# Optimization experiments

Hardware: AMD Instinct MI355X
Metric: run time of the kernel (lower is better)

The kernel has to match this reference:

```python
import jax, jax.numpy as jnp
import numpy as np

N, E, D, H, G = 50000, 800000, 128, 128, 64
EPS = 1e-5


def setup_inputs() -> dict:
    key = jax.random.key(0)
    ks = jax.random.split(key, 16)
    x = jax.random.normal(ks[0], (N, D), dtype=jnp.float32)
    edge_index = jax.random.randint(ks[1], (2, E), 0, N, dtype=jnp.int64)
    batch = jnp.sort(jax.random.randint(ks[2], (N,), 0, G, dtype=jnp.int64))
    dims = [D, H, H, H]
    params = {}
    for i in range(3):
        params[f"W{i}"] = jax.random.normal(ks[3 + i], (dims[i], dims[i + 1]), dtype=jnp.float32) * (1.0 / np.sqrt(dims[i]).astype(np.float32))
        params[f"b{i}"] = jnp.zeros((dims[i + 1],), jnp.float32)
        params[f"g{i}"] = jnp.ones((dims[i + 1],), jnp.float32)   # BN gamma
        params[f"be{i}"] = jnp.zeros((dims[i + 1],), jnp.float32)  # BN beta
    params["Wout"] = jax.random.normal(ks[10], (H, 1), dtype=jnp.float32) * (1.0 / np.sqrt(H).astype(np.float32))
    params["bout"] = jnp.zeros((1,), jnp.float32)
    return {"x": x, "edge_index": edge_index, "batch": batch, **params}


def _gcn_forward(x, edge_index, batch, Ws, bs, gs, bes, Wout, bout):
    n = x.shape[0]
    loop = jnp.arange(n)
    # GCNConv default: add self-loops, symmetric degree normalization
    src = jnp.concatenate([edge_index[0], loop])
    dst = jnp.concatenate([edge_index[1], loop])
    deg = jax.ops.segment_sum(jnp.ones_like(dst, x.dtype), dst, num_segments=n)
    dinv = jax.lax.rsqrt(jnp.maximum(deg, 1.0))  # deg >= 1 from self-loops
    norm = dinv[src] * dinv[dst]                 # [E+N]
    h = x
    for W, b, g, be in zip(Ws, bs, gs, bes):
        h = h @ W                                               # transform [N,C]
        msg = h[src] * norm[:, None]                            # gather [E+N,C]
        h = jax.ops.segment_sum(msg, dst, num_segments=n) + b   # scatter-add
        # BatchNorm1d (training-mode batch statistics over nodes)
        mu = jnp.mean(h, axis=0)
        var = jnp.var(h, axis=0)
        h = (h - mu) * jax.lax.rsqrt(var + EPS) * g + be
        h = jax.nn.relu(h)
        # dropout: identity (deterministic eval reference)
    counts = jax.ops.segment_sum(jnp.ones((n,), h.dtype), batch, num_segments=G)
    pooled = jax.ops.segment_sum(h, batch, num_segments=G) / jnp.maximum(counts, 1.0)[:, None]
    return jax.nn.sigmoid(pooled @ Wout + bout)  # [G,1]


def reference(x, edge_index, batch, W0, b0, g0, be0, W1, b1, g1, be1, W2, b2, g2, be2, Wout, bout):
    return _gcn_forward(x, edge_index, batch,
                        (W0, W1, W2), (b0, b1, b2), (g0, g1, g2), (be0, be1, be2),
                        Wout, bout)
```

## Files before the change

kernel.cpp:

```cpp
#include <hip/hip_runtime.h>

#define EPSBN 1e-5f
#define AGG_BLOCKS 2048

using bf16x8 = __attribute__((ext_vector_type(8))) short;
using f32x4  = __attribute__((ext_vector_type(4))) float;

__device__ __forceinline__ unsigned short f2bf(float f) {
    unsigned u = __builtin_bit_cast(unsigned, f);
    unsigned r = (u + 0x7FFFu + ((u >> 16) & 1u)) >> 16;
    return (unsigned short)r;
}
__device__ __forceinline__ float bf2f(unsigned short s) {
    unsigned u = ((unsigned)s) << 16;
    return __builtin_bit_cast(float, u);
}


__global__ __launch_bounds__(256) void k_bhist(const int* __restrict__ dst, int E,
                                               int* __restrict__ deg, int* __restrict__ bcnt, int shift) {
    __shared__ int lh[512];
    for (int i = threadIdx.x; i < 512; i += 256) lh[i] = 0;
    __syncthreads();
    for (int i = blockIdx.x * blockDim.x + threadIdx.x; i < E; i += gridDim.x * blockDim.x) {
        int d = dst[i];
        atomicAdd(&deg[d], 1);
        atomicAdd(&lh[d >> shift], 1);
    }
    __syncthreads();
    for (int i = threadIdx.x; i < 512; i += 256)
        if (lh[i]) atomicAdd(&bcnt[i], lh[i]);
}

__global__ void k_dinv(const int* __restrict__ deg, int N, float* __restrict__ dinv) {
    int i = blockIdx.x * blockDim.x + threadIdx.x;
    if (i < N) dinv[i] = rsqrtf((float)(deg[i] + 1));
}

__global__ void k_scan1(const int* __restrict__ deg, int N, int* __restrict__ rs, int* __restrict__ blk) {
    __shared__ int sh[256];
    int tid = threadIdx.x;
    int i = blockIdx.x * 256 + tid;
    int v = (i < N) ? deg[i] : 0;
    sh[tid] = v; __syncthreads();
    for (int off = 1; off < 256; off <<= 1) {
        int t = (tid >= off) ? sh[tid - off] : 0;
        __syncthreads();
        sh[tid] += t;
        __syncthreads();
    }
    if (i < N) rs[i] = sh[tid] - v;
    if (tid == 255) blk[blockIdx.x] = sh[255];
}

__global__ void k_scan2(const int* __restrict__ blk, int nb, int* __restrict__ blkoff) {
    __shared__ int sh[1024];
    int tid = threadIdx.x;
    int v = (tid < nb) ? blk[tid] : 0;
    sh[tid] = v; __syncthreads();
    for (int off = 1; off < 1024; off <<= 1) {
        int t = (tid >= off) ? sh[tid - off] : 0;
        __syncthreads();
        sh[tid] += t;
        __syncthreads();
    }
    if (tid < nb) blkoff[tid] = sh[tid] - v;
}

__global__ void k_scan3(int* __restrict__ rs, int N, const int* __restrict__ blkoff) {
    int i = blockIdx.x * blockDim.x + threadIdx.x;
    if (i < N) rs[i] += blkoff[i >> 8];
}


__global__ __launch_bounds__(256) void k_bscatter(const int* __restrict__ src, const int* __restrict__ dst, int E,
                                                  const int* __restrict__ boff, int* __restrict__ gcur,
                                                  uint2* __restrict__ ebuf, int shift) {
    __shared__ int lh[512], lb[512];
    int tid = threadIdx.x;
    int base = blockIdx.x * 2048;
    for (int i = tid; i < 512; i += 256) lh[i] = 0;
    __syncthreads();
    int ms[8], md[8];
    #pragma unroll
    for (int j = 0; j < 8; ++j) {
        int idx = base + j * 256 + tid;
        if (idx < E) {
            ms[j] = src[idx]; md[j] = dst[idx];
            atomicAdd(&lh[md[j] >> shift], 1);
        } else md[j] = -1;
    }
    __syncthreads();
    for (int b = tid; b < 512; b += 256) {
        int c = lh[b];
        lb[b] = c ? atomicAdd(&gcur[b], c) : 0;
    }
    __syncthreads();
    for (int i = tid; i < 512; i += 256) lh[i] = 0;
    __syncthreads();
    #pragma unroll
    for (int j = 0; j < 8; ++j) {
        if (md[j] >= 0) {
            int b = md[j] >> shift;
            int r = atomicAdd(&lh[b], 1);
            ebuf[boff[b] + lb[b] + r] = make_uint2((unsigned)ms[j], (unsigned)md[j]);
        }
    }
}


__global__ __launch_bounds__(256) void k_fill2(const uint2* __restrict__ ebuf, const int* __restrict__ bcnt,
                                               const int* __restrict__ boff, const int* __restrict__ rs,
                                               int* __restrict__ col, int shift) {
    __shared__ int lcur[256];
    int b = blockIdx.x;
    int n0 = b << shift;
    int cnt = bcnt[b], s = boff[b];
    int span = 1 << shift;
    for (int i = threadIdx.x; i < span; i += 256) lcur[i] = 0;
    __syncthreads();
    for (int i = threadIdx.x; i < cnt; i += 256) {
        uint2 e = ebuf[s + i];
        int d = (int)e.y;
        int pos = rs[d] + atomicAdd(&lcur[d - n0], 1);
        col[pos] = (int)e.x;
    }
}


__global__ __launch_bounds__(256) void k_gemm(const unsigned short* __restrict__ Abf,
                                              const float* __restrict__ Af,
                                              const float* __restrict__ W,
                                              unsigned short* __restrict__ C, int N,
                                              const float* __restrict__ scale,
                                              const float* __restrict__ shift, int mode) {
    __shared__ unsigned short Asw[128 * 128];
    __shared__ unsigned short Wt[128 * 128];
    int tid = threadIdx.x;
    int r0 = blockIdx.x * 128;

    {
        int n = tid & 127, kh = tid >> 7;
        const float* wp = &W[(kh * 64) * 128 + n];
        #pragma unroll
        for (int kb = 0; kb < 8; ++kb) {
            unsigned short t8[8];
            #pragma unroll
            for (int e = 0; e < 8; ++e)
                t8[e] = f2bf(wp[(kb * 8 + e) * 128]);
            int byte = (n * 256 + kh * 128 + kb * 16) ^ ((n & 7) << 4);
            *reinterpret_cast<uint4*>(reinterpret_cast<char*>(Wt) + byte) =
                *reinterpret_cast<const uint4*>(t8);
        }
    }
    if (mode == 0) {
        const float* ap = &Af[(size_t)r0 * 128];
        #pragma unroll
        for (int j = 0; j < 8; ++j) {
            int u = tid + j * 256;
            int row = u >> 4, cg = u & 15;
            unsigned short t8[8] = {0,0,0,0,0,0,0,0};
            if (r0 + row < N) {
                float4 a0 = *reinterpret_cast<const float4*>(ap + row * 128 + cg * 8);
                float4 a1 = *reinterpret_cast<const float4*>(ap + row * 128 + cg * 8 + 4);
                t8[0]=f2bf(a0.x); t8[1]=f2bf(a0.y); t8[2]=f2bf(a0.z); t8[3]=f2bf(a0.w);
                t8[4]=f2bf(a1.x); t8[5]=f2bf(a1.y); t8[6]=f2bf(a1.z); t8[7]=f2bf(a1.w);
            }
            int byte = (row * 256 + cg * 16) ^ ((row & 7) << 4);
            *reinterpret_cast<uint4*>(reinterpret_cast<char*>(Asw) + byte) =
                *reinterpret_cast<const uint4*>(t8);
        }
    } else {
        const unsigned short* ap = &Abf[(size_t)r0 * 128];
        #pragma unroll
        for (int j = 0; j < 8; ++j) {
            int u = tid + j * 256;
            int row = u >> 4, cg = u & 15;
            unsigned short t8[8] = {0,0,0,0,0,0,0,0};
            if (r0 + row < N) {
                ushort4 v0 = *reinterpret_cast<const ushort4*>(ap + (size_t)row * 128 + cg * 8);
                ushort4 v1 = *reinterpret_cast<const ushort4*>(ap + (size_t)row * 128 + cg * 8 + 4);
                float4 sc0 = *reinterpret_cast<const float4*>(&scale[cg * 8]);
                float4 sc1 = *reinterpret_cast<const float4*>(&scale[cg * 8 + 4]);
                float4 sf0 = *reinterpret_cast<const float4*>(&shift[cg * 8]);
                float4 sf1 = *reinterpret_cast<const float4*>(&shift[cg * 8 + 4]);
                t8[0] = f2bf(fmaxf(bf2f(v0.x) * sc0.x + sf0.x, 0.f));
                t8[1] = f2bf(fmaxf(bf2f(v0.y) * sc0.y + sf0.y, 0.f));
                t8[2] = f2bf(fmaxf(bf2f(v0.z) * sc0.z + sf0.z, 0.f));
                t8[3] = f2bf(fmaxf(bf2f(v0.w) * sc0.w + sf0.w, 0.f));
                t8[4] = f2bf(fmaxf(bf2f(v1.x) * sc1.x + sf1.x, 0.f));
                t8[5] = f2bf(fmaxf(bf2f(v1.y) * sc1.y + sf1.y, 0.f));
                t8[6] = f2bf(fmaxf(bf2f(v1.z) * sc1.z + sf1.z, 0.f));
                t8[7] = f2bf(fmaxf(bf2f(v1.w) * sc1.w + sf1.w, 0.f));
            }
            int byte = (row * 256 + cg * 16) ^ ((row & 7) << 4);
            *reinterpret_cast<uint4*>(reinterpret_cast<char*>(Asw) + byte) =
                *reinterpret_cast<const uint4*>(t8);
        }
    }
    __syncthreads();

    int wv = tid >> 6, lane = tid & 63;
    int lr = lane & 15, lk = lane >> 4;
    f32x4 acc[2][8] = {};
    #pragma unroll
    for (int kk = 0; kk < 4; ++kk) {
        bf16x8 af[2], bf[8];
        #pragma unroll
        for (int mf = 0; mf < 2; ++mf) {
            int ar = wv * 32 + mf * 16 + lr;
            int byte = (ar * 256 + kk * 64 + lk * 16) ^ ((ar & 7) << 4);
            af[mf] = *reinterpret_cast<const bf16x8*>(reinterpret_cast<const char*>(Asw) + byte);
        }
        #pragma unroll
        for (int nf = 0; nf < 8; ++nf) {
            int bn = nf * 16 + lr;
            int byte = (bn * 256 + kk * 64 + lk * 16) ^ ((bn & 7) << 4);
            bf[nf] = *reinterpret_cast<const bf16x8*>(reinterpret_cast<const char*>(Wt) + byte);
        }
        #pragma unroll
        for (int mf = 0; mf < 2; ++mf)
            #pragma unroll
            for (int nf = 0; nf < 8; ++nf)
                acc[mf][nf] = __builtin_amdgcn_mfma_f32_16x16x32_bf16(af[mf], bf[nf], acc[mf][nf], 0, 0, 0);
    }
    __syncthreads();
    #pragma unroll
    for (int mf = 0; mf < 2; ++mf)
        #pragma unroll
        for (int nf = 0; nf < 8; ++nf)
            #pragma unroll
            for (int r = 0; r < 4; ++r) {
                int row = wv * 32 + mf * 16 + lk * 4 + r;
                int colc = nf * 16 + lr;
                Asw[row * 128 + colc] = f2bf(acc[mf][nf][r]);
            }
    __syncthreads();
    #pragma unroll
    for (int j = 0; j < 8; ++j) {
        int u = tid + j * 256;
        int row = u >> 4, cg = u & 15;
        if (r0 + row < N)
            *reinterpret_cast<uint4*>(&C[((size_t)(r0 + row)) * 128 + cg * 8]) =
                *reinterpret_cast<const uint4*>(&Asw[row * 128 + cg * 8]);
    }
}


__global__ __launch_bounds__(256) void k_agg(const unsigned short* __restrict__ t, const int* __restrict__ col,
                                             const int* __restrict__ rs, const int* __restrict__ deg,
                                             const float* __restrict__ dinv, const float* __restrict__ bias,
                                             unsigned short* __restrict__ out, int N,
                                             float* __restrict__ p1, float* __restrict__ p2) {
    int wv = threadIdx.x >> 6, lane = threadIdx.x & 63;
    const ushort2* tp = reinterpret_cast<const ushort2*>(t);
    float b0 = bias[2 * lane], b1 = bias[2 * lane + 1];
    float s1x = 0.f, s1y = 0.f, s2x = 0.f, s2y = 0.f;
    for (int w = blockIdx.x * 4 + wv; w < N; w += gridDim.x * 4) {
        int start = rs[w], cnt = deg[w];
        float di = dinv[w];
        float ax = 0.f, ay = 0.f;
        int e = 0;
        for (; e + 4 <= cnt; e += 4) {
            int s0 = col[start + e], s1 = col[start + e + 1];
            int s2 = col[start + e + 2], s3 = col[start + e + 3];
            float w0 = dinv[s0], w1 = dinv[s1], w2 = dinv[s2], w3 = dinv[s3];
            ushort2 v0 = tp[(size_t)s0 * 64 + lane];
            ushort2 v1 = tp[(size_t)s1 * 64 + lane];
            ushort2 v2 = tp[(size_t)s2 * 64 + lane];
            ushort2 v3 = tp[(size_t)s3 * 64 + lane];
            ax += w0 * bf2f(v0.x) + w1 * bf2f(v1.x) + w2 * bf2f(v2.x) + w3 * bf2f(v3.x);
            ay += w0 * bf2f(v0.y) + w1 * bf2f(v1.y) + w2 * bf2f(v2.y) + w3 * bf2f(v3.y);
        }
        for (; e < cnt; ++e) {
            int s = col[start + e];
            float ww = dinv[s];
            ushort2 v = tp[(size_t)s * 64 + lane];
            ax += ww * bf2f(v.x);
            ay += ww * bf2f(v.y);
        }
        ushort2 self = tp[(size_t)w * 64 + lane];
        ushort2 o;
        o.x = f2bf(di * ax + di * di * bf2f(self.x) + b0);
        o.y = f2bf(di * ay + di * di * bf2f(self.y) + b1);
        reinterpret_cast<ushort2*>(out)[(size_t)w * 64 + lane] = o;
        float rx = bf2f(o.x), ry = bf2f(o.y);
        s1x += rx; s1y += ry; s2x += rx * rx; s2y += ry * ry;
    }
    __shared__ float sh[4][64][4];
    sh[wv][lane][0] = s1x; sh[wv][lane][1] = s1y; sh[wv][lane][2] = s2x; sh[wv][lane][3] = s2y;
    __syncthreads();
    int tid = threadIdx.x;
    if (tid < 64) {
        float a0 = 0.f, a1 = 0.f, a2 = 0.f, a3 = 0.f;
        #pragma unroll
        for (int r = 0; r < 4; ++r) {
            a0 += sh[r][tid][0]; a1 += sh[r][tid][1];
            a2 += sh[r][tid][2]; a3 += sh[r][tid][3];
        }
        p1[blockIdx.x * 128 + 2 * tid]     = a0;
        p1[blockIdx.x * 128 + 2 * tid + 1] = a1;
        p2[blockIdx.x * 128 + 2 * tid]     = a2;
        p2[blockIdx.x * 128 + 2 * tid + 1] = a3;
    }
}


__global__ __launch_bounds__(128) void k_statsmid(const float* __restrict__ p1, const float* __restrict__ p2,
                                                  int rows, float* __restrict__ pm1, float* __restrict__ pm2) {
    int c = threadIdx.x, b = blockIdx.x;
    int r0 = b * rows;
    float s1 = 0.f, s2 = 0.f;
    #pragma unroll 4
    for (int r = 0; r < rows; ++r) {
        s1 += p1[(size_t)(r0 + r) * 128 + c];
        s2 += p2[(size_t)(r0 + r) * 128 + c];
    }
    pm1[b * 128 + c] = s1;
    pm2[b * 128 + c] = s2;
}

__global__ __launch_bounds__(1024) void k_stats2(const float* __restrict__ p1, const float* __restrict__ p2,
                                                 int nb, int N,
                                                 const float* __restrict__ g, const float* __restrict__ be,
                                                 float* __restrict__ scale, float* __restrict__ shift) {
    __shared__ double sh1[1024], sh2[1024];
    int tid = threadIdx.x;
    int c = tid & 127, seg = tid >> 7;
    double s1 = 0.0, s2 = 0.0;
    int b = seg;
    for (; b + 32 <= nb; b += 32) {
        double a0 = p1[(b      ) * 128 + c], q0 = p2[(b      ) * 128 + c];
        double a1 = p1[(b +  8) * 128 + c], q1 = p2[(b +  8) * 128 + c];
        double a2 = p1[(b + 16) * 128 + c], q2 = p2[(b + 16) * 128 + c];
        double a3 = p1[(b + 24) * 128 + c], q3 = p2[(b + 24) * 128 + c];
        s1 += (a0 + a1) + (a2 + a3);
        s2 += (q0 + q1) + (q2 + q3);
    }
    for (; b < nb; b += 8) { s1 += p1[b * 128 + c]; s2 += p2[b * 128 + c]; }
    sh1[tid] = s1; sh2[tid] = s2;
    __syncthreads();
    #pragma unroll
    for (int s = 4; s >= 1; s >>= 1) {
        if (seg < s) {
            sh1[tid] += sh1[tid + s * 128];
            sh2[tid] += sh2[tid + s * 128];
        }
        __syncthreads();
    }
    if (tid < 128) {
        double mu = sh1[c] / N;
        double var = sh2[c] / N - mu * mu;
        double inv = 1.0 / sqrt(var + (double)EPSBN);
        scale[c] = (float)((double)g[c] * inv);
        shift[c] = (float)((double)be[c] - mu * (double)g[c] * inv);
    }
}


__global__ __launch_bounds__(256) void k_pool(const unsigned short* __restrict__ h, const int* __restrict__ batch,
                                              const float* __restrict__ scale, const float* __restrict__ shift,
                                              const float* __restrict__ Wout, int N, int G,
                                              float* __restrict__ pool, int* __restrict__ cnt) {
    __shared__ float pl[64];
    __shared__ int cl[64];
    int tid = threadIdx.x;
    if (tid < 64) { pl[tid] = 0.f; cl[tid] = 0; }
    __syncthreads();
    int wv = tid >> 6, lane = tid & 63;
    float sc0 = scale[2 * lane], sc1 = scale[2 * lane + 1];
    float sf0 = shift[2 * lane], sf1 = shift[2 * lane + 1];
    float w0 = Wout[2 * lane], w1 = Wout[2 * lane + 1];
    const ushort2* hp = reinterpret_cast<const ushort2*>(h);
    int wid = blockIdx.x * 4 + wv;
    int stride = gridDim.x * 4;
    for (int i = wid; i < N; i += stride * 4) {
        int i1 = i + stride, i2 = i + 2 * stride, i3 = i + 3 * stride;
        float s0 = 0.f, s1 = 0.f, s2 = 0.f, s3 = 0.f;
        {
            ushort2 v = hp[(size_t)i * 64 + lane];
            s0 = fmaxf(bf2f(v.x) * sc0 + sf0, 0.f) * w0 + fmaxf(bf2f(v.y) * sc1 + sf1, 0.f) * w1;
        }
        if (i1 < N) {
            ushort2 v = hp[(size_t)i1 * 64 + lane];
            s1 = fmaxf(bf2f(v.x) * sc0 + sf0, 0.f) * w0 + fmaxf(bf2f(v.y) * sc1 + sf1, 0.f) * w1;
        }
        if (i2 < N) {
            ushort2 v = hp[(size_t)i2 * 64 + lane];
            s2 = fmaxf(bf2f(v.x) * sc0 + sf0, 0.f) * w0 + fmaxf(bf2f(v.y) * sc1 + sf1, 0.f) * w1;
        }
        if (i3 < N) {
            ushort2 v = hp[(size_t)i3 * 64 + lane];
            s3 = fmaxf(bf2f(v.x) * sc0 + sf0, 0.f) * w0 + fmaxf(bf2f(v.y) * sc1 + sf1, 0.f) * w1;
        }
        #pragma unroll
        for (int o = 32; o > 0; o >>= 1) {
            s0 += __shfl_down(s0, o); s1 += __shfl_down(s1, o);
            s2 += __shfl_down(s2, o); s3 += __shfl_down(s3, o);
        }
        if (lane == 0) {
            atomicAdd(&pl[batch[i]], s0); atomicAdd(&cl[batch[i]], 1);
            if (i1 < N) { atomicAdd(&pl[batch[i1]], s1); atomicAdd(&cl[batch[i1]], 1); }
            if (i2 < N) { atomicAdd(&pl[batch[i2]], s2); atomicAdd(&cl[batch[i2]], 1); }
            if (i3 < N) { atomicAdd(&pl[batch[i3]], s3); atomicAdd(&cl[batch[i3]], 1); }
        }
    }
    __syncthreads();
    if (tid < 64) {
        atomicAdd(&pool[tid], pl[tid]);
        atomicAdd(&cnt[tid], cl[tid]);
    }
}

__global__ void k_final(const float* __restrict__ pool, const int* __restrict__ cnt,
                        const float* __restrict__ bout, int G, float* __restrict__ out) {
    int g = blockIdx.x * blockDim.x + threadIdx.x;
    if (g < G) {
        float c = fmaxf((float)cnt[g], 1.f);
        float p = pool[g] / c + bout[0];
        out[g] = 1.f / (1.f + expf(-p));
    }
}


extern "C" void kernel_launch(void* const* d_in, const int* in_sizes, int n_in,
                              void* d_out, int out_size, void* d_ws, size_t ws_size,
                              hipStream_t stream) {
    const float* x    = (const float*)d_in[0];
    const int*   ei   = (const int*)d_in[1];
    const int*   batch= (const int*)d_in[2];
    const float* W0p  = (const float*)d_in[3];
    const float* b0p  = (const float*)d_in[4];
    const float* g0p  = (const float*)d_in[5];
    const float* be0p = (const float*)d_in[6];
    const float* W1p  = (const float*)d_in[7];
    const float* b1p  = (const float*)d_in[8];
    const float* g1p  = (const float*)d_in[9];
    const float* be1p = (const float*)d_in[10];
    const float* W2p  = (const float*)d_in[11];
    const float* b2p  = (const float*)d_in[12];
    const float* g2p  = (const float*)d_in[13];
    const float* be2p = (const float*)d_in[14];
    const float* Woutp= (const float*)d_in[15];
    const float* boutp= (const float*)d_in[16];

    int N = in_sizes[0] / 128;
    int E = in_sizes[1] / 2;
    int G = out_size;
    const int* src = ei;
    const int* dst = ei + E;

    int shiftB = 7;
    while ((((N + (1 << shiftB) - 1) >> shiftB) > 512) && shiftB < 8) ++shiftB;
    int nbuck = (N + (1 << shiftB) - 1) >> shiftB;

    char* p = (char*)d_ws;
    auto alloc = [&](size_t bytes) {
        void* q = (void*)p;
        p += (bytes + 255) & ~(size_t)255;
        return q;
    };
    unsigned short* Bt  = (unsigned short*)alloc((size_t)N * 128 * 2);
    unsigned short* Bh  = (unsigned short*)alloc((size_t)N * 128 * 2);
    int*    col    = (int*)   alloc((size_t)E * 4);
    uint2*  ebuf   = (uint2*) alloc((size_t)E * 8);
    int*    rsA    = (int*)   alloc((size_t)N * 4);
    int*    deg    = (int*)   alloc((size_t)N * 4);
    float*  dinv   = (float*) alloc((size_t)N * 4);
    int*    blk    = (int*)   alloc(1024 * 4);
    int*    blkoff = (int*)   alloc(1024 * 4);
    int*    bcnt   = (int*)   alloc(512 * 4);
    int*    boff   = (int*)   alloc(512 * 4);
    int*    gcur   = (int*)   alloc(512 * 4);
    float*  p1     = (float*) alloc((size_t)AGG_BLOCKS * 128 * 4);
    float*  p2     = (float*) alloc((size_t)AGG_BLOCKS * 128 * 4);
    float*  pm1    = (float*) alloc(128 * 128 * 4);
    float*  pm2    = (float*) alloc(128 * 128 * 4);
    float*  scale  = (float*) alloc(128 * 4);
    float*  shift  = (float*) alloc(128 * 4);
    float*  pool   = (float*) alloc(64 * 4);
    int*    cnt    = (int*)   alloc(64 * 4);

    hipMemsetAsync(deg, 0, (size_t)N * 4, stream);
    hipMemsetAsync(bcnt, 0, 512 * 4, stream);
    hipMemsetAsync(gcur, 0, 512 * 4, stream);
    hipMemsetAsync(pool, 0, 64 * 4, stream);
    hipMemsetAsync(cnt, 0, 64 * 4, stream);

    int nb = (N + 255) / 256;
    k_bhist   <<<256, 256, 0, stream>>>(dst, E, deg, bcnt, shiftB);
    k_dinv    <<<nb, 256, 0, stream>>>(deg, N, dinv);
    k_scan1   <<<nb, 256, 0, stream>>>(deg, N, rsA, blk);
    k_scan2   <<<1, 1024, 0, stream>>>(blk, nb, blkoff);
    k_scan3   <<<nb, 256, 0, stream>>>(rsA, N, blkoff);
    k_scan2   <<<1, 1024, 0, stream>>>(bcnt, 512, boff);
    k_bscatter<<<(E + 2047) / 2048, 256, 0, stream>>>(src, dst, E, boff, gcur, ebuf, shiftB);
    k_fill2   <<<nbuck, 256, 0, stream>>>(ebuf, bcnt, boff, rsA, col, shiftB);

    int gemmBlocks = (N + 127) / 128;
    int midRows = AGG_BLOCKS / 128;

    k_gemm    <<<gemmBlocks, 256, 0, stream>>>(nullptr, x, W0p, Bt, N, scale, shift, 0);
    k_agg     <<<AGG_BLOCKS, 256, 0, stream>>>(Bt, col, rsA, deg, dinv, b0p, Bh, N, p1, p2);
    k_statsmid<<<128, 128, 0, stream>>>(p1, p2, midRows, pm1, pm2);
    k_stats2  <<<1, 1024, 0, stream>>>(pm1, pm2, 128, N, g0p, be0p, scale, shift);
    k_gemm    <<<gemmBlocks, 256, 0, stream>>>(Bh, nullptr, W1p, Bt, N, scale, shift, 1);
    k_agg     <<<AGG_BLOCKS, 256, 0, stream>>>(Bt, col, rsA, deg, dinv, b1p, Bh, N, p1, p2);
    k_statsmid<<<128, 128, 0, stream>>>(p1, p2, midRows, pm1, pm2);
    k_stats2  <<<1, 1024, 0, stream>>>(pm1, pm2, 128, N, g1p, be1p, scale, shift);
    k_gemm    <<<gemmBlocks, 256, 0, stream>>>(Bh, nullptr, W2p, Bt, N, scale, shift, 1);
    k_agg     <<<AGG_BLOCKS, 256, 0, stream>>>(Bt, col, rsA, deg, dinv, b2p, Bh, N, p1, p2);
    k_statsmid<<<128, 128, 0, stream>>>(p1, p2, midRows, pm1, pm2);
    k_stats2  <<<1, 1024, 0, stream>>>(pm1, pm2, 128, N, g2p, be2p, scale, shift);
    k_pool <<<256, 256, 0, stream>>>(Bh, batch, scale, shift, Woutp, N, G, pool, cnt);
    k_final<<<1, 64, 0, stream>>>(pool, cnt, boutp, G, (float*)d_out);
}
```

Baseline: 300.6 us.

## Pack neighbor index with dinv weight, stage edges in LDS, precompute weight images

```diff
diff --git a/kernel.cpp b/kernel.cpp
--- a/kernel.cpp
+++ b/kernel.cpp
@@ -111,7 +111,8 @@
 
 __global__ __launch_bounds__(256) void k_fill2(const uint2* __restrict__ ebuf, const int* __restrict__ bcnt,
                                                const int* __restrict__ boff, const int* __restrict__ rs,
-                                               int* __restrict__ col, int shift) {
+                                               const float* __restrict__ dinv,
+                                               uint2* __restrict__ colw, int shift) {
     __shared__ int lcur[256];
     int b = blockIdx.x;
     int n0 = b << shift;
@@ -122,15 +123,36 @@
     for (int i = threadIdx.x; i < cnt; i += 256) {
         uint2 e = ebuf[s + i];
         int d = (int)e.y;
+        int sv = (int)e.x;
         int pos = rs[d] + atomicAdd(&lcur[d - n0], 1);
-        col[pos] = (int)e.x;
+        colw[pos] = make_uint2((unsigned)sv, __builtin_bit_cast(unsigned, dinv[sv]));
+    }
+}
+
+
+__global__ __launch_bounds__(256) void k_wprep(const float* __restrict__ W0, const float* __restrict__ W1,
+                                               const float* __restrict__ W2, unsigned short* __restrict__ Wimg) {
+    const float* W = (blockIdx.x == 0) ? W0 : (blockIdx.x == 1) ? W1 : W2;
+    unsigned short* out = Wimg + (size_t)blockIdx.x * 16384;
+    int tid = threadIdx.x;
+    int n = tid & 127, kh = tid >> 7;
+    const float* wp = &W[(kh * 64) * 128 + n];
+    #pragma unroll
+    for (int kb = 0; kb < 8; ++kb) {
+        unsigned short t8[8];
+        #pragma unroll
+        for (int e = 0; e < 8; ++e)
+            t8[e] = f2bf(wp[(kb * 8 + e) * 128]);
+        int byte = (n * 256 + kh * 128 + kb * 16) ^ ((n & 7) << 4);
+        *reinterpret_cast<uint4*>(reinterpret_cast<char*>(out) + byte) =
+            *reinterpret_cast<const uint4*>(t8);
     }
 }
 
 
 __global__ __launch_bounds__(256) void k_gemm(const unsigned short* __restrict__ Abf,
                                               const float* __restrict__ Af,
-                                              const float* __restrict__ W,
+                                              const unsigned short* __restrict__ Wimg,
                                               unsigned short* __restrict__ C, int N,
                                               const float* __restrict__ scale,
                                               const float* __restrict__ shift, int mode) {
@@ -140,18 +162,11 @@
     int r0 = blockIdx.x * 128;
 
     {
-        int n = tid & 127, kh = tid >> 7;
-        const float* wp = &W[(kh * 64) * 128 + n];
-        #pragma unroll
-        for (int kb = 0; kb < 8; ++kb) {
-            unsigned short t8[8];
-            #pragma unroll
-            for (int e = 0; e < 8; ++e)
-                t8[e] = f2bf(wp[(kb * 8 + e) * 128]);
-            int byte = (n * 256 + kh * 128 + kb * 16) ^ ((n & 7) << 4);
-            *reinterpret_cast<uint4*>(reinterpret_cast<char*>(Wt) + byte) =
-                *reinterpret_cast<const uint4*>(t8);
-        }
+        const uint4* wi = reinterpret_cast<const uint4*>(Wimg);
+        uint4* wl = reinterpret_cast<uint4*>(Wt);
+        #pragma unroll
+        for (int j = 0; j < 8; ++j)
+            wl[tid + j * 256] = wi[tid + j * 256];
     }
     if (mode == 0) {
         const float* ap = &Af[(size_t)r0 * 128];
@@ -247,11 +262,13 @@
 }
 
 
-__global__ __launch_bounds__(256) void k_agg(const unsigned short* __restrict__ t, const int* __restrict__ col,
+__global__ __launch_bounds__(256) void k_agg(const unsigned short* __restrict__ t, const uint2* __restrict__ colw,
                                              const int* __restrict__ rs, const int* __restrict__ deg,
                                              const float* __restrict__ dinv, const float* __restrict__ bias,
                                              unsigned short* __restrict__ out, int N,
                                              float* __restrict__ p1, float* __restrict__ p2) {
+    __shared__ uint2 ec[4][64];
+    __shared__ float sh[4][64][4];
     int wv = threadIdx.x >> 6, lane = threadIdx.x & 63;
     const ushort2* tp = reinterpret_cast<const ushort2*>(t);
     float b0 = bias[2 * lane], b1 = bias[2 * lane + 1];
@@ -260,24 +277,29 @@
         int start = rs[w], cnt = deg[w];
         float di = dinv[w];
         float ax = 0.f, ay = 0.f;
-        int e = 0;
-        for (; e + 4 <= cnt; e += 4) {
-            int s0 = col[start + e], s1 = col[start + e + 1];
-            int s2 = col[start + e + 2], s3 = col[start + e + 3];
-            float w0 = dinv[s0], w1 = dinv[s1], w2 = dinv[s2], w3 = dinv[s3];
-            ushort2 v0 = tp[(size_t)s0 * 64 + lane];
-            ushort2 v1 = tp[(size_t)s1 * 64 + lane];
-            ushort2 v2 = tp[(size_t)s2 * 64 + lane];
-            ushort2 v3 = tp[(size_t)s3 * 64 + lane];
-            ax += w0 * bf2f(v0.x) + w1 * bf2f(v1.x) + w2 * bf2f(v2.x) + w3 * bf2f(v3.x);
-            ay += w0 * bf2f(v0.y) + w1 * bf2f(v1.y) + w2 * bf2f(v2.y) + w3 * bf2f(v3.y);
-        }
-        for (; e < cnt; ++e) {
-            int s = col[start + e];
-            float ww = dinv[s];
-            ushort2 v = tp[(size_t)s * 64 + lane];
-            ax += ww * bf2f(v.x);
-            ay += ww * bf2f(v.y);
+        for (int base = 0; base < cnt; base += 64) {
+            int m = min(cnt - base, 64);
+            if (lane < m) ec[wv][lane] = colw[start + base + lane];
+            asm volatile("s_waitcnt lgkmcnt(0)" ::: "memory");
+            int e = 0;
+            for (; e + 4 <= m; e += 4) {
+                uint2 e0 = ec[wv][e], e1 = ec[wv][e + 1], e2 = ec[wv][e + 2], e3 = ec[wv][e + 3];
+                ushort2 v0 = tp[(size_t)e0.x * 64 + lane];
+                ushort2 v1 = tp[(size_t)e1.x * 64 + lane];
+                ushort2 v2 = tp[(size_t)e2.x * 64 + lane];
+                ushort2 v3 = tp[(size_t)e3.x * 64 + lane];
+                float w0 = __builtin_bit_cast(float, e0.y), w1 = __builtin_bit_cast(float, e1.y);
+                float w2 = __builtin_bit_cast(float, e2.y), w3 = __builtin_bit_cast(float, e3.y);
+                ax += w0 * bf2f(v0.x) + w1 * bf2f(v1.x) + w2 * bf2f(v2.x) + w3 * bf2f(v3.x);
+                ay += w0 * bf2f(v0.y) + w1 * bf2f(v1.y) + w2 * bf2f(v2.y) + w3 * bf2f(v3.y);
+            }
+            for (; e < m; ++e) {
+                uint2 ee = ec[wv][e];
+                ushort2 v = tp[(size_t)ee.x * 64 + lane];
+                float ww = __builtin_bit_cast(float, ee.y);
+                ax += ww * bf2f(v.x);
+                ay += ww * bf2f(v.y);
+            }
         }
         ushort2 self = tp[(size_t)w * 64 + lane];
         ushort2 o;
@@ -287,7 +309,6 @@
         float rx = bf2f(o.x), ry = bf2f(o.y);
         s1x += rx; s1y += ry; s2x += rx * rx; s2y += ry * ry;
     }
-    __shared__ float sh[4][64][4];
     sh[wv][lane][0] = s1x; sh[wv][lane][1] = s1y; sh[wv][lane][2] = s2x; sh[wv][lane][3] = s2y;
     __syncthreads();
     int tid = threadIdx.x;
@@ -462,7 +483,7 @@
     };
     unsigned short* Bt  = (unsigned short*)alloc((size_t)N * 128 * 2);
     unsigned short* Bh  = (unsigned short*)alloc((size_t)N * 128 * 2);
-    int*    col    = (int*)   alloc((size_t)E * 4);
+    uint2*  colw   = (uint2*) alloc((size_t)E * 8);
     uint2*  ebuf   = (uint2*) alloc((size_t)E * 8);
     int*    rsA    = (int*)   alloc((size_t)N * 4);
     int*    deg    = (int*)   alloc((size_t)N * 4);
@@ -472,6 +493,7 @@
     int*    bcnt   = (int*)   alloc(512 * 4);
     int*    boff   = (int*)   alloc(512 * 4);
     int*    gcur   = (int*)   alloc(512 * 4);
+    unsigned short* Wimg = (unsigned short*)alloc(3 * 16384 * 2);
     float*  p1     = (float*) alloc((size_t)AGG_BLOCKS * 128 * 4);
     float*  p2     = (float*) alloc((size_t)AGG_BLOCKS * 128 * 4);
     float*  pm1    = (float*) alloc(128 * 128 * 4);
@@ -488,6 +510,7 @@
     hipMemsetAsync(cnt, 0, 64 * 4, stream);
 
     int nb = (N + 255) / 256;
+    k_wprep   <<<3, 256, 0, stream>>>(W0p, W1p, W2p, Wimg);
     k_bhist   <<<256, 256, 0, stream>>>(dst, E, deg, bcnt, shiftB);
     k_dinv    <<<nb, 256, 0, stream>>>(deg, N, dinv);
     k_scan1   <<<nb, 256, 0, stream>>>(deg, N, rsA, blk);
@@ -495,21 +518,21 @@
     k_scan3   <<<nb, 256, 0, stream>>>(rsA, N, blkoff);
     k_scan2   <<<1, 1024, 0, stream>>>(bcnt, 512, boff);
     k_bscatter<<<(E + 2047) / 2048, 256, 0, stream>>>(src, dst, E, boff, gcur, ebuf, shiftB);
-    k_fill2   <<<nbuck, 256, 0, stream>>>(ebuf, bcnt, boff, rsA, col, shiftB);
+    k_fill2   <<<nbuck, 256, 0, stream>>>(ebuf, bcnt, boff, rsA, dinv, colw, shiftB);
 
     int gemmBlocks = (N + 127) / 128;
     int midRows = AGG_BLOCKS / 128;
 
-    k_gemm    <<<gemmBlocks, 256, 0, stream>>>(nullptr, x, W0p, Bt, N, scale, shift, 0);
-    k_agg     <<<AGG_BLOCKS, 256, 0, stream>>>(Bt, col, rsA, deg, dinv, b0p, Bh, N, p1, p2);
+    k_gemm    <<<gemmBlocks, 256, 0, stream>>>(nullptr, x, Wimg, Bt, N, scale, shift, 0);
+    k_agg     <<<AGG_BLOCKS, 256, 0, stream>>>(Bt, colw, rsA, deg, dinv, b0p, Bh, N, p1, p2);
     k_statsmid<<<128, 128, 0, stream>>>(p1, p2, midRows, pm1, pm2);
     k_stats2  <<<1, 1024, 0, stream>>>(pm1, pm2, 128, N, g0p, be0p, scale, shift);
-    k_gemm    <<<gemmBlocks, 256, 0, stream>>>(Bh, nullptr, W1p, Bt, N, scale, shift, 1);
-    k_agg     <<<AGG_BLOCKS, 256, 0, stream>>>(Bt, col, rsA, deg, dinv, b1p, Bh, N, p1, p2);
+    k_gemm    <<<gemmBlocks, 256, 0, stream>>>(Bh, nullptr, Wimg + 16384, Bt, N, scale, shift, 1);
+    k_agg     <<<AGG_BLOCKS, 256, 0, stream>>>(Bt, colw, rsA, deg, dinv, b1p, Bh, N, p1, p2);
     k_statsmid<<<128, 128, 0, stream>>>(p1, p2, midRows, pm1, pm2);
     k_stats2  <<<1, 1024, 0, stream>>>(pm1, pm2, 128, N, g1p, be1p, scale, shift);
-    k_gemm    <<<gemmBlocks, 256, 0, stream>>>(Bh, nullptr, W2p, Bt, N, scale, shift, 1);
-    k_agg     <<<AGG_BLOCKS, 256, 0, stream>>>(Bt, col, rsA, deg, dinv, b2p, Bh, N, p1, p2);
+    k_gemm    <<<gemmBlocks, 256, 0, stream>>>(Bh, nullptr, Wimg + 32768, Bt, N, scale, shift, 1);
+    k_agg     <<<AGG_BLOCKS, 256, 0, stream>>>(Bt, colw, rsA, deg, dinv, b2p, Bh, N, p1, p2);
     k_statsmid<<<128, 128, 0, stream>>>(p1, p2, midRows, pm1, pm2);
     k_stats2  <<<1, 1024, 0, stream>>>(pm1, pm2, 128, N, g2p, be2p, scale, shift);
     k_pool <<<256, 256, 0, stream>>>(Bh, batch, scale, shift, Woutp, N, G, pool, cnt);
```

Measured after the change: 290.4 us. 3.4% less time.
